# Kernel optimization log

Hardware: AMD Instinct MI355X
Metric: run time of the kernel (lower is better)

The kernel has to match this reference:

```python
import math
import jax, jax.numpy as jnp
import numpy as np

B, T, C = 2, 2048, 1024
H, HKV, HD = 16, 4, 64  # n_head, n_kv_head, head_dim
G = H // HKV            # GQA groups
WS = 1024               # sliding window size
GATE_CH = 32


def setup_inputs() -> dict:
    key = jax.random.key(0)
    ks = jax.random.split(key, 8)
    x = jax.random.normal(ks[0], (B, T, C), dtype=jnp.float32)
    ve = jax.random.normal(ks[1], (B, T, HKV * HD), dtype=jnp.float32)
    # realistic RoPE tables: half head_dim frequencies
    d = HD // 2
    inv_freq = 1.0 / (10000.0 ** (jnp.arange(d, dtype=jnp.float32) / d))
    angles = jnp.arange(T, dtype=jnp.float32)[:, None] * inv_freq[None, :]  # (T, d)
    cos = jnp.cos(angles)[None, :, None, :]  # (1, T, 1, d)
    sin = jnp.sin(angles)[None, :, None, :]
    s = 0.02
    Wq = s * jax.random.normal(ks[2], (C, H * HD), dtype=jnp.float32)
    Wk = s * jax.random.normal(ks[3], (C, HKV * HD), dtype=jnp.float32)
    Wv = s * jax.random.normal(ks[4], (C, HKV * HD), dtype=jnp.float32)
    Wproj = s * jax.random.normal(ks[5], (C, C), dtype=jnp.float32)
    Wg = s * jax.random.normal(ks[6], (GATE_CH, HKV), dtype=jnp.float32)
    return {"x": x, "ve": ve, "cos": cos, "sin": sin,
            "Wq": Wq, "Wk": Wk, "Wv": Wv, "Wproj": Wproj, "Wg": Wg, "ws": WS}


def _rope(u, cos, sin):
    d = u.shape[-1] // 2
    u1, u2 = u[..., :d], u[..., d:]
    return jnp.concatenate([u1 * cos + u2 * sin, -u1 * sin + u2 * cos], axis=-1)


def _rmsnorm(u):
    eps = jnp.finfo(u.dtype).eps
    return u * jax.lax.rsqrt(jnp.mean(u * u, axis=-1, keepdims=True) + eps)


def reference(x, ve, cos, sin, Wq, Wk, Wv, Wproj, Wg, ws):
    b, t, c = x.shape
    q = (x @ Wq).reshape(b, t, H, HD)
    k = (x @ Wk).reshape(b, t, HKV, HD)
    v = (x @ Wv).reshape(b, t, HKV, HD)
    # value-embedding gate: 2*sigmoid over first 32 channels of x
    gate = 2.0 * jax.nn.sigmoid(x[..., :GATE_CH] @ Wg)  # (b, t, HKV)
    v = v + gate[..., None] * ve.reshape(b, t, HKV, HD)
    q = _rmsnorm(_rope(q, cos, sin))
    k = _rmsnorm(_rope(k, cos, sin))
    # GQA: view q as (b, t, HKV, G, HD), contract against shared k/v per kv-head
    qg = q.reshape(b, t, HKV, G, HD)
    scale = 1.0 / math.sqrt(HD)
    scores = jnp.einsum('bqhgd,bkhd->bhgqk', qg, k) * scale  # (b, HKV, G, t, t)
    pos = jnp.arange(t)
    # key j attends iff i - ws + 1 <= j <= i (sliding causal window)
    mask = (pos[None, :] >= pos[:, None] - ws + 1) & (pos[None, :] <= pos[:, None])
    scores = jnp.where(mask[None, None, None], scores, -jnp.inf)
    attn = jax.nn.softmax(scores, axis=-1)
    y = jnp.einsum('bhgqk,bkhd->bqhgd', attn, v).reshape(b, t, H * HD)
    return y @ Wproj
```

## Files before the change

### kernel.cpp

```cpp
#include <hip/hip_runtime.h>
#include <hip/hip_bf16.h>

#define Bq 2
#define Tq 2048
#define Cq 1024
#define Hq 16
#define HKVq 4
#define HDq 64
#define Gq 4
#define WSq 1024
#define GATE_CHq 32

typedef __attribute__((ext_vector_type(8))) short short8;
typedef __attribute__((ext_vector_type(4))) float f32x4;
typedef __attribute__((ext_vector_type(2))) unsigned int u32x2;
typedef unsigned int u32;
typedef unsigned short u16;

#if __has_builtin(__builtin_amdgcn_exp2f)
#define EXP2(x) __builtin_amdgcn_exp2f(x)
#else
#define EXP2(x) exp2f(x)
#endif

__device__ __forceinline__ u16 f2bf(float f) {
  u32 u = __float_as_uint(f);
  u32 r = (u + 0x7FFFu + ((u >> 16) & 1u)) >> 16;
  return (u16)r;
}
__device__ __forceinline__ float bf2f(u16 u) {
  return __uint_as_float(((u32)u) << 16);
}

__device__ __forceinline__ void gl_lds16(const u16* g, u16* l) {
  __builtin_amdgcn_global_load_lds(
      (const u32 __attribute__((address_space(1)))*)g,
      (u32 __attribute__((address_space(3)))*)l, 16, 0, 0);
}

__global__ __launch_bounds__(256) void qkv_gemm_fused(
    const u16* __restrict__ A, const u16* __restrict__ Bt,
    const float* __restrict__ ve, const float* __restrict__ cosp,
    const float* __restrict__ sinp, const float* __restrict__ gatebuf,
    u16* __restrict__ Qb, u16* __restrict__ Kb, u16* __restrict__ Vtb) {
  __shared__ __attribute__((aligned(16))) u16 As[64 * 64];
  __shared__ __attribute__((aligned(16))) u16 Bs[128 * 64];

  const int bx = blockIdx.x;
  const int bm0 = blockIdx.y * 64, bn0 = bx * 128;
  const int tid = threadIdx.x;
  const int w = tid >> 6, lane = tid & 63;
  const int wm = (w >> 1) * 32, wn = (w & 1) * 64;
  const int quad = lane >> 4, l16 = lane & 15;
  const int K = 1024;

  f32x4 acc[2][4];
#pragma unroll
  for (int mt = 0; mt < 2; mt++)
#pragma unroll
    for (int nt = 0; nt < 4; nt++) acc[mt][nt] = (f32x4){0.f, 0.f, 0.f, 0.f};

  int goffA[2], goffB[4];
#pragma unroll
  for (int i = 0; i < 2; i++) {
    int s = i * 256 + tid;
    int m = s >> 3, gp = s & 7;
    goffA[i] = m * K + (gp ^ (m & 7)) * 8;
  }
#pragma unroll
  for (int i = 0; i < 4; i++) {
    int s = i * 256 + tid;
    int m = s >> 3, gp = s & 7;
    goffB[i] = m * K + (gp ^ (m & 7)) * 8;
  }
  const u16* Ab = A + (long)bm0 * K;
  const u16* Bb = Bt + (long)bn0 * K;

  for (int k0 = 0; k0 < K; k0 += 64) {
    __syncthreads();
#pragma unroll
    for (int i = 0; i < 2; i++)
      gl_lds16(Ab + goffA[i] + k0, &As[(i * 256 + w * 64) * 8]);
#pragma unroll
    for (int i = 0; i < 4; i++)
      gl_lds16(Bb + goffB[i] + k0, &Bs[(i * 256 + w * 64) * 8]);
    __syncthreads();

#pragma unroll
    for (int ks = 0; ks < 2; ks++) {
      short8 af[2], bf[4];
#pragma unroll
      for (int mt = 0; mt < 2; mt++) {
        int ml = wm + mt * 16 + l16;
        af[mt] = *(const short8*)&As[ml * 64 + (((ks * 4 + quad) ^ (ml & 7)) * 8)];
      }
#pragma unroll
      for (int nt = 0; nt < 4; nt++) {
        int nl = wn + nt * 16 + l16;
        bf[nt] = *(const short8*)&Bs[nl * 64 + (((ks * 4 + quad) ^ (nl & 7)) * 8)];
      }
#pragma unroll
      for (int mt = 0; mt < 2; mt++)
#pragma unroll
        for (int nt = 0; nt < 4; nt++)
          acc[mt][nt] = __builtin_amdgcn_mfma_f32_16x16x32_bf16(
              af[mt], bf[nt], acc[mt][nt], 0, 0, 0);
    }
  }

  const int b = bm0 >> 11;
  const int tseq0 = (bm0 & 2047) + wm;

  if (bx < 10) {
    u16* Dst;
    if (bx < 8) {
      int hh = bx * 2 + (w & 1);
      int hkv = hh >> 2, g = hh & 3;
      Dst = Qb + ((long)((b * 4 + hkv) * 4 + g) * Tq) * 64;
    } else {
      int kk = (bx - 8) * 2 + (w & 1);
      Dst = Kb + ((long)(b * 4 + kk) * Tq) * 64;
    }
#pragma unroll
    for (int mt = 0; mt < 2; mt++) {
#pragma unroll
      for (int r = 0; r < 4; r++) {
        int t = tseq0 + mt * 16 + quad * 4 + r;
        float c0 = cosp[t * 32 + l16];
        float s0 = sinp[t * 32 + l16];
        float c1 = cosp[t * 32 + 16 + l16];
        float s1 = sinp[t * 32 + 16 + l16];
        float a0 = acc[mt][0][r], a1 = acc[mt][1][r];
        float a2 = acc[mt][2][r], a3 = acc[mt][3][r];
        float rp0 = a0 * c0 + a2 * s0;
        float rp1 = a1 * c1 + a3 * s1;
        float rp2 = a2 * c0 - a0 * s0;
        float rp3 = a3 * c1 - a1 * s1;
        float ss = rp0 * rp0 + rp1 * rp1 + rp2 * rp2 + rp3 * rp3;
        ss += __shfl_xor(ss, 1);
        ss += __shfl_xor(ss, 2);
        ss += __shfl_xor(ss, 4);
        ss += __shfl_xor(ss, 8);
        float sc = rsqrtf(ss * (1.f / 64.f) + 1.1920928955078125e-07f);
        u16* drow = Dst + (long)t * 64;
        drow[l16] = f2bf(rp0 * sc);
        drow[16 + l16] = f2bf(rp1 * sc);
        drow[32 + l16] = f2bf(rp2 * sc);
        drow[48 + l16] = f2bf(rp3 * sc);
      }
    }
  } else {
    int kk = (bx - 10) * 2 + (w & 1);
    u16* Dst = Vtb + ((long)(b * 4 + kk) * 64) * Tq;
#pragma unroll
    for (int mt = 0; mt < 2; mt++) {
      float vals[4][4];
#pragma unroll
      for (int r = 0; r < 4; r++) {
        int t = tseq0 + mt * 16 + quad * 4 + r;
        long bt = (long)b * Tq + t;
        float gv = gatebuf[bt * 4 + kk];
        const float* verow = ve + bt * 256 + kk * 64;
#pragma unroll
        for (int nt = 0; nt < 4; nt++)
          vals[nt][r] = acc[mt][nt][r] + gv * verow[nt * 16 + l16];
      }
      int t0m = tseq0 + mt * 16 + quad * 4;
#pragma unroll
      for (int nt = 0; nt < 4; nt++) {
        int d = nt * 16 + l16;
        union { short4 v; u16 u[4]; } p;
#pragma unroll
        for (int r = 0; r < 4; r++) p.u[r] = f2bf(vals[nt][r]);
        *(short4*)(Dst + (long)d * Tq + t0m) = p.v;
      }
    }
  }
}

__global__ __launch_bounds__(256) void gemm_proj(
    const u16* __restrict__ A, const u16* __restrict__ Bt,
    float* __restrict__ C, int M, int N, int K) {
  __shared__ __attribute__((aligned(16))) u16 As[64 * 64];
  __shared__ __attribute__((aligned(16))) u16 Bs[128 * 64];

  const int bm0 = blockIdx.y * 64, bn0 = blockIdx.x * 128;
  const int tid = threadIdx.x;
  const int w = tid >> 6, lane = tid & 63;
  const int wm = (w >> 1) * 32, wn = (w & 1) * 64;
  const int quad = lane >> 4, l16 = lane & 15;

  f32x4 acc[2][4];
#pragma unroll
  for (int mt = 0; mt < 2; mt++)
#pragma unroll
    for (int nt = 0; nt < 4; nt++) acc[mt][nt] = (f32x4){0.f, 0.f, 0.f, 0.f};

  int goffA[2], goffB[4];
#pragma unroll
  for (int i = 0; i < 2; i++) {
    int s = i * 256 + tid;
    int m = s >> 3, gp = s & 7;
    goffA[i] = m * K + (gp ^ (m & 7)) * 8;
  }
#pragma unroll
  for (int i = 0; i < 4; i++) {
    int s = i * 256 + tid;
    int m = s >> 3, gp = s & 7;
    goffB[i] = m * K + (gp ^ (m & 7)) * 8;
  }
  const u16* Ab = A + (long)bm0 * K;
  const u16* Bb = Bt + (long)bn0 * K;

  for (int k0 = 0; k0 < K; k0 += 64) {
    __syncthreads();
#pragma unroll
    for (int i = 0; i < 2; i++)
      gl_lds16(Ab + goffA[i] + k0, &As[(i * 256 + w * 64) * 8]);
#pragma unroll
    for (int i = 0; i < 4; i++)
      gl_lds16(Bb + goffB[i] + k0, &Bs[(i * 256 + w * 64) * 8]);
    __syncthreads();

#pragma unroll
    for (int ks = 0; ks < 2; ks++) {
      short8 af[2], bf[4];
#pragma unroll
      for (int mt = 0; mt < 2; mt++) {
        int ml = wm + mt * 16 + l16;
        af[mt] = *(const short8*)&As[ml * 64 + (((ks * 4 + quad) ^ (ml & 7)) * 8)];
      }
#pragma unroll
      for (int nt = 0; nt < 4; nt++) {
        int nl = wn + nt * 16 + l16;
        bf[nt] = *(const short8*)&Bs[nl * 64 + (((ks * 4 + quad) ^ (nl & 7)) * 8)];
      }
#pragma unroll
      for (int mt = 0; mt < 2; mt++)
#pragma unroll
        for (int nt = 0; nt < 4; nt++)
          acc[mt][nt] = __builtin_amdgcn_mfma_f32_16x16x32_bf16(
              af[mt], bf[nt], acc[mt][nt], 0, 0, 0);
    }
  }

#pragma unroll
  for (int mt = 0; mt < 2; mt++)
#pragma unroll
    for (int nt = 0; nt < 4; nt++) {
      int row0 = bm0 + wm + mt * 16 + quad * 4;
      int col = bn0 + wn + nt * 16 + l16;
#pragma unroll
      for (int r = 0; r < 4; r++)
        C[(long)(row0 + r) * N + col] = acc[mt][nt][r];
    }
}

__global__ __launch_bounds__(256) void prep(
    const float* __restrict__ x, u16* __restrict__ xb,
    const float* __restrict__ Wq, const float* __restrict__ Wk,
    const float* __restrict__ Wv, const float* __restrict__ Wproj,
    const float* __restrict__ Wg, u16* __restrict__ Dqkv,
    u16* __restrict__ Dproj, float* __restrict__ gatebuf) {
  __shared__ float tile[64][65];
  int bx = blockIdx.x;
  int tid = threadIdx.x;
  if (bx < 2048) {
    int i = (bx * 256 + tid) * 8;
    float4 a = *(const float4*)(x + i);
    float4 b = *(const float4*)(x + i + 4);
    union { short8 v; u16 u[8]; } o;
    o.u[0] = f2bf(a.x); o.u[1] = f2bf(a.y); o.u[2] = f2bf(a.z); o.u[3] = f2bf(a.w);
    o.u[4] = f2bf(b.x); o.u[5] = f2bf(b.y); o.u[6] = f2bf(b.z); o.u[7] = f2bf(b.w);
    *(short8*)(xb + i) = o.v;
    return;
  }
  if (bx >= 2688) {
    int p = (bx - 2688) * 256 + tid;
    int bt = p >> 2, kk = p & 3;
    const float* xr = x + (long)bt * Cq;
    float dot = 0.f;
#pragma unroll
    for (int i = 0; i < GATE_CHq; i++) dot += xr[i] * Wg[i * HKVq + kk];
    gatebuf[p] = 2.f / (1.f + expf(-dot));
    return;
  }
  int wb = bx - 2048;
  int obx = wb >> 4;
  int k0 = (wb & 15) * 64;
  const float* S;
  u16* Dst;
  int N, nb;
  if (obx < 16)      { S = Wq;    N = 1024; nb = obx;      Dst = Dqkv; }
  else if (obx < 20) { S = Wk;    N = 256;  nb = obx - 16; Dst = Dqkv + 1024 * 1024; }
  else if (obx < 24) { S = Wv;    N = 256;  nb = obx - 20; Dst = Dqkv + 1280 * 1024; }
  else               { S = Wproj; N = 1024; nb = obx - 24; Dst = Dproj; }
  int n0 = nb * 64;
#pragma unroll
  for (int i = 0; i < 16; i++) {
    int idx = i * 256 + tid;
    int kl = idx >> 6, nl = idx & 63;
    tile[kl][nl] = S[(long)(k0 + kl) * N + n0 + nl];
  }
  __syncthreads();
#pragma unroll
  for (int i = 0; i < 16; i++) {
    int idx = i * 256 + tid;
    int nl = idx >> 6, kl = idx & 63;
    Dst[(long)(n0 + nl) * 1024 + k0 + kl] = f2bf(tile[kl][nl]);
  }
}

#define CEXP 0.18033688011112042f
#define CEXP8 1.4426950408889634f

template <bool MASK>
__device__ __forceinline__ void attn_chunk(
    int k0, int q0, int quad, int l16, const u16* __restrict__ kf_addr,
    const u16* __restrict__ vf_addr, u32* __restrict__ myPs,
    const short8 (&QB)[2][2], f32x4 (&O)[2][4], float (&lsum)[2]) {
  short8 kf[4][2];
#pragma unroll
  for (int kt4 = 0; kt4 < 4; kt4++) {
    kf[kt4][0] = *(const short8*)(kf_addr + kt4 * 1024);
    kf[kt4][1] = *(const short8*)(kf_addr + kt4 * 1024 + 32);
  }
  short8 vf[4][2];
#pragma unroll
  for (int nt = 0; nt < 4; nt++) {
    vf[nt][0] = *(const short8*)(vf_addr + (long)nt * 16 * Tq);
    vf[nt][1] = *(const short8*)(vf_addr + (long)nt * 16 * Tq + 32);
  }

  f32x4 S4[4][2];
#pragma unroll
  for (int kt4 = 0; kt4 < 4; kt4++)
#pragma unroll
    for (int qj = 0; qj < 2; qj++) {
      f32x4 acc = (f32x4){0.f, 0.f, 0.f, 0.f};
      acc = __builtin_amdgcn_mfma_f32_16x16x32_bf16(kf[kt4][0], QB[qj][0], acc,
                                                    0, 0, 0);
      acc = __builtin_amdgcn_mfma_f32_16x16x32_bf16(kf[kt4][1], QB[qj][1], acc,
                                                    0, 0, 0);
      S4[kt4][qj] = acc;
    }

#pragma unroll
  for (int kt4 = 0; kt4 < 4; kt4++)
#pragma unroll
    for (int qj = 0; qj < 2; qj++) {
      float Pv[4];
#pragma unroll
      for (int r = 0; r < 4; r++) {
        float sv = S4[kt4][qj][r];
        if (MASK) {
          int kpos = k0 + kt4 * 16 + quad * 4 + r;
          int qpos = q0 + qj * 16 + l16;
          bool valid = (kpos <= qpos) && (kpos >= qpos - (WSq - 1));
          sv = valid ? sv : -1e30f;
        }
        float p = EXP2(__builtin_fmaf(sv, CEXP, -CEXP8));
        Pv[r] = p;
        lsum[qj] += p;
      }
      u32x2 pk;
#pragma unroll
      for (int rp = 0; rp < 2; rp++) {
        u32 lo = __float_as_uint(Pv[2 * rp]) + 0x8000u;
        u32 hi = __float_as_uint(Pv[2 * rp + 1]) + 0x8000u;
        pk[rp] = __builtin_amdgcn_perm(hi, lo, 0x07060302u);
      }
      *(u32x2*)(&myPs[(qj * 16 + l16) * 36 + kt4 * 8 + quad * 2]) = pk;
    }

#pragma unroll
  for (int qj = 0; qj < 2; qj++) {
    const u32* prow = &myPs[(qj * 16 + l16) * 36];
    short8 pa0 = *(const short8*)(prow + quad * 4);
    short8 pa1 = *(const short8*)(prow + 16 + quad * 4);
#pragma unroll
    for (int nt = 0; nt < 4; nt++) {
      O[qj][nt] =
          __builtin_amdgcn_mfma_f32_16x16x32_bf16(pa0, vf[nt][0], O[qj][nt], 0, 0, 0);
      O[qj][nt] =
          __builtin_amdgcn_mfma_f32_16x16x32_bf16(pa1, vf[nt][1], O[qj][nt], 0, 0, 0);
    }
  }
}

__global__ __launch_bounds__(256, 3) void attn_mfma(
    const u16* __restrict__ Qb, const u16* __restrict__ Kb,
    const u16* __restrict__ Vtb, u16* __restrict__ Yb) {
  __shared__ __attribute__((aligned(16))) u32 Ps[4][32 * 36];

  int bid = blockIdx.x;
  int bh = bid & 7;
  int qt32 = bid >> 3;
  int hkv = bh & 3;
  int b = bh >> 2;
  int q0 = qt32 * 32;
  int tid = threadIdx.x;
  int g = tid >> 6;
  int lane = tid & 63;
  int quad = lane >> 4;
  int l16 = lane & 15;

  short8 QB[2][2];
#pragma unroll
  for (int qj = 0; qj < 2; qj++) {
    const u16* qb =
        Qb + ((long)((bh * 4 + g) * Tq + q0 + qj * 16 + l16)) * 64 + quad * 8;
    QB[qj][0] = *(const short8*)(qb);
    QB[qj][1] = *(const short8*)(qb + 32);
  }

  f32x4 O[2][4];
#pragma unroll
  for (int qj = 0; qj < 2; qj++)
#pragma unroll
    for (int nt = 0; nt < 4; nt++) O[qj][nt] = (f32x4){0.f, 0.f, 0.f, 0.f};
  float lsum[2] = {0.f, 0.f};

  int lo = q0 - (WSq - 1);
  int k0s = (lo < 0 ? 0 : lo) & ~63;
  int k0e = q0 & ~63;

  const u16* Kbase = Kb + ((long)bh * Tq) * 64;
  const u16* Vbase = Vtb + ((long)bh * 64) * Tq;
  u32* myPs = &Ps[g][0];

  const u16* kf_addr = Kbase + (long)(k0s + l16) * 64 + quad * 8;
  const u16* vf_addr = Vbase + (long)l16 * Tq + k0s + quad * 8;

  int k0 = k0s;
  if (q0 >= WSq && k0 < k0e) {
    attn_chunk<true>(k0, q0, quad, l16, kf_addr, vf_addr, myPs, QB, O, lsum);
    k0 += 64;
    kf_addr += 64 * 64;
    vf_addr += 64;
  }
  for (; k0 < k0e; k0 += 64) {
    attn_chunk<false>(k0, q0, quad, l16, kf_addr, vf_addr, myPs, QB, O, lsum);
    kf_addr += 64 * 64;
    vf_addr += 64;
  }
  attn_chunk<true>(k0, q0, quad, l16, kf_addr, vf_addr, myPs, QB, O, lsum);

#pragma unroll
  for (int qj = 0; qj < 2; qj++) {
    lsum[qj] += __shfl_xor(lsum[qj], 16);
    lsum[qj] += __shfl_xor(lsum[qj], 32);
  }

  int h = hkv * 4 + g;
#pragma unroll
  for (int qj = 0; qj < 2; qj++) {
    float invl[4];
#pragma unroll
    for (int r = 0; r < 4; r++) invl[r] = 1.f / __shfl(lsum[qj], quad * 4 + r);
#pragma unroll
    for (int nt = 0; nt < 4; nt++)
#pragma unroll
      for (int r = 0; r < 4; r++)
        Yb[((long)(b * Tq + q0 + qj * 16 + quad * 4 + r)) * 1024 + h * 64 +
           nt * 16 + l16] = f2bf(O[qj][nt][r] * invl[r]);
  }
}

extern "C" void kernel_launch(void* const* d_in, const int* in_sizes, int n_in,
                              void* d_out, int out_size, void* d_ws,
                              size_t ws_size, hipStream_t stream) {
  const float* x     = (const float*)d_in[0];
  const float* ve    = (const float*)d_in[1];
  const float* cosp  = (const float*)d_in[2];
  const float* sinp  = (const float*)d_in[3];
  const float* Wq    = (const float*)d_in[4];
  const float* Wk    = (const float*)d_in[5];
  const float* Wv    = (const float*)d_in[6];
  const float* Wproj = (const float*)d_in[7];
  const float* Wg    = (const float*)d_in[8];

  char* base = (char*)d_ws;
  u16* xb      = (u16*)(base);
  u16* Yb      = xb;
  u16* WqkvT   = (u16*)(base + 8388608);
  u16* WprojT  = (u16*)(base + 11534336);
  u16* Qb      = (u16*)(base + 13631488);
  u16* Kb      = (u16*)(base + 22020096);
  u16* Vtb     = (u16*)(base + 24117248);
  float* gateb = (float*)(base + 26214400);
  float* out = (float*)d_out;

  prep<<<2752, 256, 0, stream>>>(x, xb, Wq, Wk, Wv, Wproj, Wg, WqkvT, WprojT,
                                 gateb);
  qkv_gemm_fused<<<dim3(12, 64), 256, 0, stream>>>(xb, WqkvT, ve, cosp, sinp,
                                                   gateb, Qb, Kb, Vtb);
  attn_mfma<<<512, 256, 0, stream>>>(Qb, Kb, Vtb, Yb);
  gemm_proj<<<dim3(8, 64), 256, 0, stream>>>(Yb, WprojT, out, 4096, 1024, 1024);
}
```

Baseline: 193.6 us.

## Double-buffer K/V register fragments in attention loop to prefetch next chunk

New measurement: 270.7 us. 1.4x slower.

```diff
diff --git a/kernel.cpp b/kernel.cpp
--- a/kernel.cpp
+++ b/kernel.cpp
@@ -314,24 +314,29 @@
 #define CEXP 0.18033688011112042f
 #define CEXP8 1.4426950408889634f
 
+__device__ __forceinline__ void load_kv(const u16* __restrict__ kf_base,
+                                        const u16* __restrict__ vf_base,
+                                        int k0, short8 (&kf)[4][2],
+                                        short8 (&vf)[4][2]) {
+  const u16* ka = kf_base + (long)k0 * 64;
+  const u16* va = vf_base + k0;
+#pragma unroll
+  for (int kt4 = 0; kt4 < 4; kt4++) {
+    kf[kt4][0] = *(const short8*)(ka + kt4 * 1024);
+    kf[kt4][1] = *(const short8*)(ka + kt4 * 1024 + 32);
+  }
+#pragma unroll
+  for (int nt = 0; nt < 4; nt++) {
+    vf[nt][0] = *(const short8*)(va + (long)nt * 16 * Tq);
+    vf[nt][1] = *(const short8*)(va + (long)nt * 16 * Tq + 32);
+  }
+}
+
 template <bool MASK>
 __device__ __forceinline__ void attn_chunk(
-    int k0, int q0, int quad, int l16, const u16* __restrict__ kf_addr,
-    const u16* __restrict__ vf_addr, u32* __restrict__ myPs,
-    const short8 (&QB)[2][2], f32x4 (&O)[2][4], float (&lsum)[2]) {
-  short8 kf[4][2];
-#pragma unroll
-  for (int kt4 = 0; kt4 < 4; kt4++) {
-    kf[kt4][0] = *(const short8*)(kf_addr + kt4 * 1024);
-    kf[kt4][1] = *(const short8*)(kf_addr + kt4 * 1024 + 32);
-  }
-  short8 vf[4][2];
-#pragma unroll
-  for (int nt = 0; nt < 4; nt++) {
-    vf[nt][0] = *(const short8*)(vf_addr + (long)nt * 16 * Tq);
-    vf[nt][1] = *(const short8*)(vf_addr + (long)nt * 16 * Tq + 32);
-  }
-
+    int k0, int q0, int quad, int l16, const short8 (&kf)[4][2],
+    const short8 (&vf)[4][2], u32* __restrict__ myPs, const short8 (&QB)[2][2],
+    f32x4 (&O)[2][4], float (&lsum)[2]) {
   f32x4 S4[4][2];
 #pragma unroll
   for (int kt4 = 0; kt4 < 4; kt4++)
@@ -388,7 +393,7 @@
   }
 }
 
-__global__ __launch_bounds__(256, 3) void attn_mfma(
+__global__ __launch_bounds__(256, 2) void attn_mfma(
     const u16* __restrict__ Qb, const u16* __restrict__ Kb,
     const u16* __restrict__ Vtb, u16* __restrict__ Yb) {
   __shared__ __attribute__((aligned(16))) u32 Ps[4][32 * 36];
@@ -425,26 +430,55 @@
   int k0s = (lo < 0 ? 0 : lo) & ~63;
   int k0e = q0 & ~63;
 
-  const u16* Kbase = Kb + ((long)bh * Tq) * 64;
-  const u16* Vbase = Vtb + ((long)bh * 64) * Tq;
+  const u16* kf_base = Kb + ((long)bh * Tq) * 64 + (long)l16 * 64 + quad * 8;
+  const u16* vf_base = Vtb + ((long)bh * 64) * Tq + (long)l16 * Tq + quad * 8;
   u32* myPs = &Ps[g][0];
 
-  const u16* kf_addr = Kbase + (long)(k0s + l16) * 64 + quad * 8;
-  const u16* vf_addr = Vbase + (long)l16 * Tq + k0s + quad * 8;
-
+  short8 kfA[4][2], vfA[4][2], kfB[4][2], vfB[4][2];
   int k0 = k0s;
+  load_kv(kf_base, vf_base, k0, kfA, vfA);
+
   if (q0 >= WSq && k0 < k0e) {
-    attn_chunk<true>(k0, q0, quad, l16, kf_addr, vf_addr, myPs, QB, O, lsum);
+    load_kv(kf_base, vf_base, k0 + 64, kfB, vfB);
+    attn_chunk<true>(k0, q0, quad, l16, kfA, vfA, myPs, QB, O, lsum);
     k0 += 64;
-    kf_addr += 64 * 64;
-    vf_addr += 64;
-  }
-  for (; k0 < k0e; k0 += 64) {
-    attn_chunk<false>(k0, q0, quad, l16, kf_addr, vf_addr, myPs, QB, O, lsum);
-    kf_addr += 64 * 64;
-    vf_addr += 64;
-  }
-  attn_chunk<true>(k0, q0, quad, l16, kf_addr, vf_addr, myPs, QB, O, lsum);
+    while (k0 < k0e) {
+      load_kv(kf_base, vf_base, k0 + 64, kfA, vfA);
+      attn_chunk<false>(k0, q0, quad, l16, kfB, vfB, myPs, QB, O, lsum);
+      k0 += 64;
+      if (k0 == k0e) {
+        attn_chunk<true>(k0, q0, quad, l16, kfA, vfA, myPs, QB, O, lsum);
+        goto done;
+      }
+      load_kv(kf_base, vf_base, k0 + 64, kfB, vfB);
+      attn_chunk<false>(k0, q0, quad, l16, kfA, vfA, myPs, QB, O, lsum);
+      k0 += 64;
+      if (k0 == k0e) {
+        attn_chunk<true>(k0, q0, quad, l16, kfB, vfB, myPs, QB, O, lsum);
+        goto done;
+      }
+    }
+    attn_chunk<true>(k0, q0, quad, l16, kfB, vfB, myPs, QB, O, lsum);
+    goto done;
+  }
+  while (k0 < k0e) {
+    load_kv(kf_base, vf_base, k0 + 64, kfB, vfB);
+    attn_chunk<false>(k0, q0, quad, l16, kfA, vfA, myPs, QB, O, lsum);
+    k0 += 64;
+    if (k0 == k0e) {
+      attn_chunk<true>(k0, q0, quad, l16, kfB, vfB, myPs, QB, O, lsum);
+      goto done;
+    }
+    load_kv(kf_base, vf_base, k0 + 64, kfA, vfA);
+    attn_chunk<false>(k0, q0, quad, l16, kfB, vfB, myPs, QB, O, lsum);
+    k0 += 64;
+    if (k0 == k0e) {
+      attn_chunk<true>(k0, q0, quad, l16, kfA, vfA, myPs, QB, O, lsum);
+      goto done;
+    }
+  }
+  attn_chunk<true>(k0, q0, quad, l16, kfA, vfA, myPs, QB, O, lsum);
+done:
 
 #pragma unroll
   for (int qj = 0; qj < 2; qj++) {
```
